# Kernel optimization log

Measured on AMD Instinct MI355X. Metric: run time of the kernel, lower is better.

## Reference

```python
import jax, jax.numpy as jnp
import numpy as np

HIDDEN = 1024
JOINTS = 21
IN_DIM = JOINTS * 3  # 63
BATCH = 64
SEQ = 512


def setup_inputs() -> dict:
    key = jax.random.key(0)
    ks = jax.random.split(key, 11)
    s = 0.02
    f32 = jnp.float32
    return {
        "real_seq": jax.random.normal(ks[0], (BATCH, SEQ, IN_DIM), f32),
        # PyTorch nn.GRU params (gates ordered r, z, n)
        "W_ih": jax.random.normal(ks[1], (3 * HIDDEN, IN_DIM), f32) * s,
        "W_hh": jax.random.normal(ks[2], (3 * HIDDEN, HIDDEN), f32) * s,
        "b_ih": jax.random.normal(ks[3], (3 * HIDDEN,), f32) * s,
        "b_hh": jax.random.normal(ks[4], (3 * HIDDEN,), f32) * s,
        # projector MLP (no nonlinearities in the original)
        "W1": jax.random.normal(ks[5], (HIDDEN, HIDDEN), f32) * s,
        "b1": jax.random.normal(ks[6], (HIDDEN,), f32) * s,
        "W2": jax.random.normal(ks[7], (HIDDEN, HIDDEN), f32) * s,
        "b2": jax.random.normal(ks[8], (HIDDEN,), f32) * s,
        "W3": jax.random.normal(ks[9], (IN_DIM, HIDDEN), f32) * s,
        "b3": jax.random.normal(ks[10], (IN_DIM,), f32) * s,
        "condition_length": 5,
        "ground_truth_length": 5,
    }


def _condition_list(seq_len, condition_length, ground_truth_length):
    gt = np.ones((100, ground_truth_length))
    co = np.zeros((100, condition_length))
    return np.concatenate((gt, co), 1).reshape(-1)[:seq_len]


def reference(real_seq, W_ih, W_hh, b_ih, b_hh, W1, b1, W2, b2, W3, b3,
              condition_length, ground_truth_length):
    B, T, D = real_seq.shape
    H = W_hh.shape[1]
    cond = jnp.asarray(_condition_list(T, condition_length, ground_truth_length),
                       dtype=real_seq.dtype)  # [T], static 1/0 teacher-forcing pattern

    h0 = jnp.zeros((B, H), real_seq.dtype)
    o0 = jnp.zeros((B, D), real_seq.dtype)
    xs = (jnp.transpose(real_seq, (1, 0, 2)), cond)  # time-major

    def step(carry, x):
        h, out = carry
        xt, c = x
        inp = jnp.where(c > 0.5, xt, out)  # teacher-forcing switch
        gi = inp @ W_ih.T + b_ih           # [B, 3H]
        gh = h @ W_hh.T + b_hh             # [B, 3H]
        i_r, i_z, i_n = jnp.split(gi, 3, axis=-1)
        h_r, h_z, h_n = jnp.split(gh, 3, axis=-1)
        r = jax.nn.sigmoid(i_r + h_r)
        z = jax.nn.sigmoid(i_z + h_z)
        n = jnp.tanh(i_n + r * h_n)
        h_new = (1.0 - z) * n + z * h
        lin = (h_new @ W1.T + b1) @ W2.T + b2
        out_new = inp + lin @ W3.T + b3    # residual velocities
        return (h_new, out_new), out_new

    _, outs = jax.lax.scan(step, (h0, o0), xs)  # outs: [T, B, D]
    return jnp.transpose(outs, (1, 0, 2)).reshape(B, T, D // 3, 3)
```

## Files before the change

### kernel.cpp

```cpp
#include <hip/hip_runtime.h>
#include <hip/hip_bf16.h>


#define HIDDEN 1024
#define INDIM  63
#define TSEQ   512
#define MB     16
#define NGRP   4
#define HB_DW  (MB * 512)

typedef __attribute__((ext_vector_type(8))) short bfrag8;
typedef __attribute__((ext_vector_type(4))) float ffrag4;
typedef __attribute__((ext_vector_type(4))) unsigned u32x4;
typedef unsigned long long ull;

#define MFMA_B16(a, b, c) __builtin_amdgcn_mfma_f32_16x16x32_bf16((a), (b), (c), 0, 0, 0)

#define GLOAD4(dst, ptr) \
  asm volatile("global_load_dwordx4 %0, %1, off sc0 sc1" \
               : "=v"(dst) : "v"(ptr) : "memory")

__device__ __forceinline__ short f2bf(float x) {
  __hip_bfloat16 b = __float2bfloat16(x);
  return __builtin_bit_cast(short, b);
}
__device__ __forceinline__ float bf2f(short s) {
  unsigned u = ((unsigned)(unsigned short)s) << 16;
  return __builtin_bit_cast(float, u);
}


__global__ void k_t1(const float* __restrict__ W2, const float* __restrict__ b1,
                     const float* __restrict__ b2, float* __restrict__ t1) {
  const int w = threadIdx.x >> 6, lane = threadIdx.x & 63;
  const int o = blockIdx.x * 4 + w;
  if (o >= HIDDEN) return;
  const float* row = W2 + (size_t)o * HIDDEN;
  float s = 0.f;
  for (int k = lane; k < HIDDEN; k += 64) s += row[k] * b1[k];
  for (int off = 32; off; off >>= 1) s += __shfl_down(s, off, 64);
  if (lane == 0) t1[o] = s + b2[o];
}

__global__ void k_bp(const float* __restrict__ W3, const float* __restrict__ t1,
                     const float* __restrict__ b3, float* __restrict__ bp) {
  const int w = threadIdx.x >> 6, lane = threadIdx.x & 63;
  for (int d = w; d < INDIM; d += 4) {
    const float* row = W3 + (size_t)d * HIDDEN;
    float s = 0.f;
    for (int k = lane; k < HIDDEN; k += 64) s += row[k] * t1[k];
    for (int off = 32; off; off >>= 1) s += __shfl_down(s, off, 64);
    if (lane == 0) bp[d] = s + b3[d];
  }
}

__global__ void k_gemm(const float* __restrict__ A, const float* __restrict__ B,
                       float* __restrict__ C, int M, int N, int K) {
  __shared__ float As[16][17], Bs[16][17];
  const int tx = threadIdx.x, ty = threadIdx.y;
  const int row = blockIdx.y * 16 + ty;
  const int col = blockIdx.x * 16 + tx;
  float acc = 0.f;
  for (int k0 = 0; k0 < K; k0 += 16) {
    As[ty][tx] = (row < M) ? A[(size_t)row * K + k0 + tx] : 0.f;
    Bs[ty][tx] = B[(size_t)(k0 + ty) * N + col];
    __syncthreads();
#pragma unroll
    for (int kk = 0; kk < 16; ++kk) acc += As[ty][kk] * Bs[kk][tx];
    __syncthreads();
  }
  if (row < M && col < N) C[(size_t)row * N + col] = acc;
}


__global__ __launch_bounds__(256, 1) void k_main(
    const float* __restrict__ X,
    const float* __restrict__ W_ih, const float* __restrict__ W_hh,
    const float* __restrict__ b_ih, const float* __restrict__ b_hh,
    const float* __restrict__ WpF, const float* __restrict__ bpF,
    const int* __restrict__ pCL, const int* __restrict__ pGT,
    unsigned* __restrict__ hb, unsigned* __restrict__ fl,
    float* __restrict__ OUT) {
  __shared__ short h_st[MB][HIDDEN + 8];
  __shared__ short inp_bf[MB][88];
  __shared__ float inp_f[MB][68];
  __shared__ float gt_z[MB][20], gt_hn[MB][20];
  __shared__ float gt_ir[MB][20], gt_iz[MB][20], gt_in[MB][20];
  __shared__ short htmp[MB][20];

  const int tid = threadIdx.x;
  const int w = tid >> 6;
  const int lane = tid & 63;
  const int c = lane & 15;
  const int quad = lane >> 4;
  const int g = blockIdx.x >> 6;
  const int j = blockIdx.x & 63;

  const int gtv = pGT[0];
  int period = pCL[0] + gtv;
  if (period < 1) period = 1;

  bfrag8 wB[32];
  bfrag8 wp[32];
  if (w < 3) {
    const float* wr = W_hh + ((size_t)w * HIDDEN + (size_t)j * 16 + c) * HIDDEN;
#pragma unroll
    for (int ks = 0; ks < 32; ++ks) {
      const float* p = wr + ks * 32 + quad * 8;
      bfrag8 f;
#pragma unroll
      for (int e = 0; e < 8; ++e) f[e] = f2bf(p[e]);
      wB[ks] = f;
    }
  } else {
#pragma unroll
    for (int gate = 0; gate < 3; ++gate) {
      const float* wr = W_ih + ((size_t)gate * HIDDEN + (size_t)j * 16 + c) * INDIM;
#pragma unroll
      for (int ks = 0; ks < 2; ++ks) {
        bfrag8 f;
#pragma unroll
        for (int e = 0; e < 8; ++e) {
          int k = ks * 32 + quad * 8 + e;
          f[e] = (k < INDIM) ? f2bf(wr[k]) : (short)0;
        }
        wB[gate * 2 + ks] = f;
      }
    }
  }
  const int dd = 16 * w + c;
  {
    const float* wr = WpF + (size_t)dd * HIDDEN;
#pragma unroll
    for (int ks = 0; ks < 32; ++ks) {
      bfrag8 f;
#pragma unroll
      for (int e = 0; e < 8; ++e)
        f[e] = (dd < INDIM) ? f2bf(wr[ks * 32 + quad * 8 + e]) : (short)0;
      wp[ks] = f;
    }
  }

  float bias_g;
  if (w == 0)      bias_g = b_ih[j * 16 + c] + b_hh[j * 16 + c];
  else if (w == 1) bias_g = b_ih[HIDDEN + j * 16 + c] + b_hh[HIDDEN + j * 16 + c];
  else if (w == 2) bias_g = b_hh[2 * HIDDEN + j * 16 + c];
  else             bias_g = b_ih[2 * HIDDEN + j * 16 + c];
  const float bp_l = (dd < INDIM) ? bpF[dd] : 0.f;

  for (int i = tid; i < MB * (HIDDEN + 8); i += 256) ((short*)h_st)[i] = 0;
  for (int i = tid; i < MB * 88; i += 256) ((short*)inp_bf)[i] = 0;
  for (int i = tid; i < MB * 68; i += 256) ((float*)inp_f)[i] = 0.f;

  unsigned* hb_g[2] = {hb + (size_t)g * HB_DW,
                       hb + (size_t)(NGRP + g) * HB_DW};
  unsigned* fg = fl + g * 64;
  const unsigned* fladdr = fg + (lane & 15) * 4;

  const int xrow = tid >> 4, xd0 = (tid & 15) * 4;
  float xp[4];
  if ((0 % period) < gtv) {
    const float* xr = X + ((size_t)(g * MB + xrow) * TSEQ + 0) * INDIM;
#pragma unroll
    for (int e = 0; e < 4; ++e) xp[e] = (xd0 + e < INDIM) ? xr[xd0 + e] : 0.f;
  }

  for (int t = 0; t < TSEQ; ++t) {
    const unsigned tg = (unsigned)(t + 1);
    const bool teach = ((t % period) < gtv);
    if (teach) {
#pragma unroll
      for (int e = 0; e < 4; ++e) {
        inp_f[xrow][xd0 + e] = xp[e];
        inp_bf[xrow][xd0 + e] = f2bf(xp[e]);
      }
    }
    __syncthreads();

    ffrag4 ghr;
    float hp[4];
    if (w < 3) {
      ffrag4 acc[4];
#pragma unroll
      for (int e = 0; e < 4; ++e) {
        acc[0][e] = bias_g; acc[1][e] = 0.f; acc[2][e] = 0.f; acc[3][e] = 0.f;
      }
#pragma unroll
      for (int ks = 0; ks < 32; ++ks) {
        const bfrag8 a = *(const bfrag8*)&h_st[c][ks * 32 + quad * 8];
        acc[ks & 3] = MFMA_B16(a, wB[ks], acc[ks & 3]);
      }
      ffrag4 gsum = acc[0] + acc[1] + acc[2] + acc[3];
      if (w == 1) {
#pragma unroll
        for (int i = 0; i < 4; ++i) gt_z[quad * 4 + i][c] = gsum[i];
      } else if (w == 2) {
#pragma unroll
        for (int i = 0; i < 4; ++i) gt_hn[quad * 4 + i][c] = gsum[i];
      } else {
        ghr = gsum;
#pragma unroll
        for (int i = 0; i < 4; ++i) hp[i] = bf2f(h_st[quad * 4 + i][j * 16 + c]);
      }
    } else {
      ffrag4 gir, giz, gin;
#pragma unroll
      for (int e = 0; e < 4; ++e) { gir[e] = 0.f; giz[e] = 0.f; gin[e] = bias_g; }
#pragma unroll
      for (int ks = 0; ks < 2; ++ks) {
        const bfrag8 a = *(const bfrag8*)&inp_bf[c][ks * 32 + quad * 8];
        gir = MFMA_B16(a, wB[0 + ks], gir);
        giz = MFMA_B16(a, wB[2 + ks], giz);
        gin = MFMA_B16(a, wB[4 + ks], gin);
      }
#pragma unroll
      for (int i = 0; i < 4; ++i) {
        gt_ir[quad * 4 + i][c] = gir[i];
        gt_iz[quad * 4 + i][c] = giz[i];
        gt_in[quad * 4 + i][c] = gin[i];
      }
    }
    __syncthreads();

    unsigned* hw = hb_g[t & 1];
    if (w == 0) {
#pragma unroll
      for (int i = 0; i < 4; ++i) {
        const int row = quad * 4 + i;
        float r = 1.f / (1.f + __expf(-(ghr[i] + gt_ir[row][c])));
        float z = 1.f / (1.f + __expf(-(gt_z[row][c] + gt_iz[row][c])));
        float n = tanhf(gt_in[row][c] + r * gt_hn[row][c]);
        htmp[row][c] = f2bf((1.f - z) * n + z * hp[i]);
      }
      asm volatile("" ::: "memory");
      const int r = lane >> 2, li = lane & 3, q4 = li * 4;
      ull pv = (ull)(unsigned short)htmp[r][q4 + 0] |
               ((ull)(unsigned short)htmp[r][q4 + 1] << 16) |
               ((ull)(unsigned short)htmp[r][q4 + 2] << 32) |
               ((ull)(unsigned short)htmp[r][q4 + 3] << 48);
      __hip_atomic_store((ull*)hw + (size_t)r * 256 + j * 4 + li, pv,
                         __ATOMIC_RELAXED, __HIP_MEMORY_SCOPE_SYSTEM);
      asm volatile("s_waitcnt vmcnt(0)" ::: "memory");
      if (lane == 0)
        __hip_atomic_store(&fg[j], tg, __ATOMIC_RELAXED,
                           __HIP_MEMORY_SCOPE_SYSTEM);
    }

    {
      const int tn = t + 1;
      if (tn < TSEQ && ((tn % period) < gtv)) {
        const float* xr = X + ((size_t)(g * MB + xrow) * TSEQ + tn) * INDIM;
#pragma unroll
        for (int e = 0; e < 4; ++e) xp[e] = (xd0 + e < INDIM) ? xr[xd0 + e] : 0.f;
      }
    }

    {
      for (;;) {
        u32x4 fv;
        GLOAD4(fv, fladdr);
        asm volatile("s_waitcnt vmcnt(0)" ::: "memory");
        __builtin_amdgcn_sched_barrier(0);
        const bool ok = fv[0] >= tg && fv[1] >= tg && fv[2] >= tg && fv[3] >= tg;
        if (__ballot(!ok) == 0ull) break;
        __builtin_amdgcn_s_sleep(1);
      }

      u32x4 v[8];
      const unsigned* gp = hw;
#pragma unroll
      for (int s = 0; s < 8; ++s) GLOAD4(v[s], gp + (size_t)(s * 256 + tid) * 4);
      asm volatile("s_waitcnt vmcnt(0)" ::: "memory");
      __builtin_amdgcn_sched_barrier(0);
#pragma unroll
      for (int s = 0; s < 8; ++s) {
        const int u = s * 256 + tid;
        const int row = u >> 7;
        const int col0 = (u & 127) * 8;
        *(u32x4*)&h_st[row][col0] = v[s];
      }
    }
    __syncthreads();

    const int wj = t & 63;
    const bool rep = (t + 1 < TSEQ) && !(((t + 1) % period) < gtv);
    if (rep || j == wj) {
      ffrag4 oa0, oa1;
#pragma unroll
      for (int e = 0; e < 4; ++e) { oa0[e] = bp_l; oa1[e] = 0.f; }
#pragma unroll
      for (int ks = 0; ks < 32; ++ks) {
        const bfrag8 a = *(const bfrag8*)&h_st[c][ks * 32 + quad * 8];
        if (ks & 1) oa1 = MFMA_B16(a, wp[ks], oa1);
        else        oa0 = MFMA_B16(a, wp[ks], oa0);
      }
      ffrag4 o = oa0 + oa1;
#pragma unroll
      for (int i = 0; i < 4; ++i) {
        const int row = quad * 4 + i;
        if (dd < INDIM) {
          float val = o[i] + inp_f[row][dd];
          if (j == wj) OUT[((size_t)(g * MB + row) * TSEQ + t) * INDIM + dd] = val;
          if (rep) { inp_f[row][dd] = val; inp_bf[row][dd] = f2bf(val); }
        } else if (rep) {
          inp_bf[row][dd] = 0;
        }
      }
    }
  }
}


extern "C" void kernel_launch(void* const* d_in, const int* in_sizes, int n_in,
                              void* d_out, int out_size, void* d_ws, size_t ws_size,
                              hipStream_t stream) {
  const float* X    = (const float*)d_in[0];
  const float* W_ih = (const float*)d_in[1];
  const float* W_hh = (const float*)d_in[2];
  const float* b_ih = (const float*)d_in[3];
  const float* b_hh = (const float*)d_in[4];
  const float* W1   = (const float*)d_in[5];
  const float* b1   = (const float*)d_in[6];
  const float* W2   = (const float*)d_in[7];
  const float* b2   = (const float*)d_in[8];
  const float* W3   = (const float*)d_in[9];
  const float* b3   = (const float*)d_in[10];
  const int* pCL    = (const int*)d_in[11];
  const int* pGT    = (const int*)d_in[12];
  float* OUT = (float*)d_out;

  char* ws = (char*)d_ws;
  float* bp = (float*)(ws + 1024);
  float* t1 = (float*)(ws + 2048);
  float* Wp = (float*)(ws + 8192);
  float* T2 = (float*)(ws + 270336);
  unsigned* hb = (unsigned*)(ws + 270336);
  unsigned* fl = (unsigned*)(ws + 270336 + 2 * NGRP * HB_DW * sizeof(unsigned));
  if (ws_size < 795 * 1024) return;

  k_t1<<<256, 256, 0, stream>>>(W2, b1, b2, t1);
  k_gemm<<<dim3(64, 4), dim3(16, 16), 0, stream>>>(W3, W2, T2, INDIM, HIDDEN, HIDDEN);
  k_gemm<<<dim3(64, 4), dim3(16, 16), 0, stream>>>(T2, W1, Wp, INDIM, HIDDEN, HIDDEN);
  k_bp<<<1, 256, 0, stream>>>(W3, t1, b3, bp);
  hipMemsetAsync(hb, 0,
                 (size_t)2 * NGRP * HB_DW * sizeof(unsigned) +
                     NGRP * 64 * sizeof(unsigned),
                 stream);
  k_main<<<256, 256, 0, stream>>>(X, W_ih, W_hh, b_ih, b_hh, Wp, bp, pCL, pGT,
                                  hb, fl, OUT);
}
```

Baseline: 3.483 ms.

## Split batch into eight groups and add XCD-local fast sync path with fallback

Result: slower. 12.75 ms (+266.0%).

```diff
diff --git a/kernel.cpp b/kernel.cpp
--- a/kernel.cpp
+++ b/kernel.cpp
@@ -5,20 +5,17 @@
 #define HIDDEN 1024
 #define INDIM  63
 #define TSEQ   512
-#define MB     16
-#define NGRP   4
-#define HB_DW  (MB * 512)
+#define MB     8
+#define GROUPS 8
+#define PAYDW  4096
 
 typedef __attribute__((ext_vector_type(8))) short bfrag8;
 typedef __attribute__((ext_vector_type(4))) float ffrag4;
 typedef __attribute__((ext_vector_type(4))) unsigned u32x4;
+typedef __attribute__((ext_vector_type(2))) unsigned u32x2;
 typedef unsigned long long ull;
 
 #define MFMA_B16(a, b, c) __builtin_amdgcn_mfma_f32_16x16x32_bf16((a), (b), (c), 0, 0, 0)
-
-#define GLOAD4(dst, ptr) \
-  asm volatile("global_load_dwordx4 %0, %1, off sc0 sc1" \
-               : "=v"(dst) : "v"(ptr) : "memory")
 
 __device__ __forceinline__ short f2bf(float x) {
   __hip_bfloat16 b = __float2bfloat16(x);
@@ -73,37 +70,68 @@
 }
 
 
-__global__ __launch_bounds__(256, 1) void k_main(
+__global__ __launch_bounds__(512, 2) void k_main(
     const float* __restrict__ X,
     const float* __restrict__ W_ih, const float* __restrict__ W_hh,
     const float* __restrict__ b_ih, const float* __restrict__ b_hh,
     const float* __restrict__ WpF, const float* __restrict__ bpF,
     const int* __restrict__ pCL, const int* __restrict__ pGT,
-    unsigned* __restrict__ hb, unsigned* __restrict__ fl,
-    float* __restrict__ OUT) {
-  __shared__ short h_st[MB][HIDDEN + 8];
-  __shared__ short inp_bf[MB][88];
-  __shared__ float inp_f[MB][68];
-  __shared__ float gt_z[MB][20], gt_hn[MB][20];
-  __shared__ float gt_ir[MB][20], gt_iz[MB][20], gt_in[MB][20];
-  __shared__ short htmp[MB][20];
+    unsigned* __restrict__ ctrl, unsigned* __restrict__ hbM,
+    unsigned* __restrict__ hbF, float* __restrict__ OUT) {
+  __shared__ short h_st[16][HIDDEN + 8];
+  __shared__ short inp_bf[16][88];
+  __shared__ float inp_f[16][68];
+  __shared__ float gt_z[2][16][20], gt_hn[2][16][20];
+  __shared__ float gt_ir[2][16][20], gt_iz[2][16][20], gt_in[2][16][20];
+  __shared__ short htmp[2][16][20];
 
   const int tid = threadIdx.x;
-  const int w = tid >> 6;
+  const int w8 = tid >> 6;
   const int lane = tid & 63;
+  const int sl = w8 >> 2;
+  const int ww = w8 & 3;
   const int c = lane & 15;
   const int quad = lane >> 4;
-  const int g = blockIdx.x >> 6;
-  const int j = blockIdx.x & 63;
+  const int bid = blockIdx.x;
+  const int g = bid & 7;
+  const int blockj = bid >> 3;
+  const int js = blockj * 2 + sl;
+
+  unsigned* flM = ctrl;
+  unsigned* xa  = ctrl + 512;
+  unsigned* vt  = ctrl + 768;
+  unsigned* dg  = ctrl + 1024;
+  unsigned* pw  = ctrl + 1056;
+  ull* ebc      = (ull*)(ctrl + 1344);
+  ull* flF      = (ull*)(ctrl + 1376);
+  ull* epoch    = (ull*)(ctrl + 2400);
+
+  unsigned* flMg = flM + g * 64;
+  ull*      flFg = flF + g * 64;
+  unsigned* dgg  = dg + g;
+
+  if (tid == 0) {
+    unsigned* pp = pw + g * 32 + blockj;
+    unsigned mk = 0xA5u;
+    asm volatile("global_store_dword %0, %1, off sc0" :: "v"(pp), "v"(mk) : "memory");
+    asm volatile("s_waitcnt vmcnt(0)" ::: "memory");
+    __hip_atomic_store(xa + g * 32 + blockj, 1u, __ATOMIC_RELAXED,
+                       __HIP_MEMORY_SCOPE_SYSTEM);
+    if (bid == 0) {
+      ull e = __hip_atomic_fetch_add(epoch, 1ull, __ATOMIC_RELAXED,
+                                     __HIP_MEMORY_SCOPE_SYSTEM);
+      __hip_atomic_store(ebc, (e << 1) | 1ull, __ATOMIC_RELAXED,
+                         __HIP_MEMORY_SCOPE_SYSTEM);
+    }
+  }
 
   const int gtv = pGT[0];
   int period = pCL[0] + gtv;
   if (period < 1) period = 1;
 
   bfrag8 wB[32];
-  bfrag8 wp[32];
-  if (w < 3) {
-    const float* wr = W_hh + ((size_t)w * HIDDEN + (size_t)j * 16 + c) * HIDDEN;
+  if (ww < 3) {
+    const float* wr = W_hh + ((size_t)ww * HIDDEN + (size_t)js * 16 + c) * HIDDEN;
 #pragma unroll
     for (int ks = 0; ks < 32; ++ks) {
       const float* p = wr + ks * 32 + quad * 8;
@@ -115,7 +143,7 @@
   } else {
 #pragma unroll
     for (int gate = 0; gate < 3; ++gate) {
-      const float* wr = W_ih + ((size_t)gate * HIDDEN + (size_t)j * 16 + c) * INDIM;
+      const float* wr = W_ih + ((size_t)gate * HIDDEN + (size_t)js * 16 + c) * INDIM;
 #pragma unroll
       for (int ks = 0; ks < 2; ++ks) {
         bfrag8 f;
@@ -128,8 +156,9 @@
       }
     }
   }
-  const int dd = 16 * w + c;
-  {
+  const int dd = 16 * w8 + c;
+  bfrag8 wp[32];
+  if (w8 < 4) {
     const float* wr = WpF + (size_t)dd * HIDDEN;
 #pragma unroll
     for (int ks = 0; ks < 32; ++ks) {
@@ -142,24 +171,60 @@
   }
 
   float bias_g;
-  if (w == 0)      bias_g = b_ih[j * 16 + c] + b_hh[j * 16 + c];
-  else if (w == 1) bias_g = b_ih[HIDDEN + j * 16 + c] + b_hh[HIDDEN + j * 16 + c];
-  else if (w == 2) bias_g = b_hh[2 * HIDDEN + j * 16 + c];
-  else             bias_g = b_ih[2 * HIDDEN + j * 16 + c];
-  const float bp_l = (dd < INDIM) ? bpF[dd] : 0.f;
-
-  for (int i = tid; i < MB * (HIDDEN + 8); i += 256) ((short*)h_st)[i] = 0;
-  for (int i = tid; i < MB * 88; i += 256) ((short*)inp_bf)[i] = 0;
-  for (int i = tid; i < MB * 68; i += 256) ((float*)inp_f)[i] = 0.f;
-
-  unsigned* hb_g[2] = {hb + (size_t)g * HB_DW,
-                       hb + (size_t)(NGRP + g) * HB_DW};
-  unsigned* fg = fl + g * 64;
-  const unsigned* fladdr = fg + (lane & 15) * 4;
+  if (ww == 0)      bias_g = b_ih[js * 16 + c] + b_hh[js * 16 + c];
+  else if (ww == 1) bias_g = b_ih[HIDDEN + js * 16 + c] + b_hh[HIDDEN + js * 16 + c];
+  else if (ww == 2) bias_g = b_hh[2 * HIDDEN + js * 16 + c];
+  else              bias_g = b_ih[2 * HIDDEN + js * 16 + c];
+  const float bp_l = (w8 < 4 && dd < INDIM) ? bpF[dd] : 0.f;
+
+  for (int i = tid; i < 16 * (HIDDEN + 8); i += 512) ((short*)h_st)[i] = 0;
+  for (int i = tid; i < 16 * 88; i += 512) ((short*)inp_bf)[i] = 0;
+  for (int i = tid; i < 16 * 68; i += 512) ((float*)inp_f)[i] = 0.f;
+
+  {
+    const unsigned* a = xa + g * 32 + (lane & 31);
+    while (__hip_atomic_load(a, __ATOMIC_RELAXED, __HIP_MEMORY_SCOPE_SYSTEM) == 0)
+      __builtin_amdgcn_s_sleep(2);
+  }
+  if (tid < 64) {
+    const unsigned* pp = pw + g * 32 + (lane & 31);
+    int okp = 0;
+    for (int it = 0; it < 64; ++it) {
+      unsigned v;
+      asm volatile("global_load_dword %0, %1, off sc0" : "=v"(v) : "v"(pp) : "memory");
+      asm volatile("s_waitcnt vmcnt(0)" ::: "memory");
+      __builtin_amdgcn_sched_barrier(0);
+      if (__ballot(v == 0) == 0ull) { okp = 1; break; }
+      __builtin_amdgcn_s_sleep(2);
+    }
+    if (lane == 0)
+      __hip_atomic_store(vt + g * 32 + blockj, okp ? 1u : 2u,
+                         __ATOMIC_RELAXED, __HIP_MEMORY_SCOPE_SYSTEM);
+  }
+  bool fast;
+  {
+    const unsigned* vv = vt + g * 32 + (lane & 31);
+    unsigned mv;
+    while ((mv = __hip_atomic_load(vv, __ATOMIC_RELAXED,
+                                   __HIP_MEMORY_SCOPE_SYSTEM)) == 0)
+      __builtin_amdgcn_s_sleep(2);
+    fast = (__ballot(mv != 1u) == 0ull);
+  }
+  ull ftg_base;
+  {
+    ull e;
+    while (((e = __hip_atomic_load(ebc, __ATOMIC_RELAXED,
+                                   __HIP_MEMORY_SCOPE_SYSTEM)) & 1ull) == 0)
+      __builtin_amdgcn_s_sleep(2);
+    ftg_base = (e >> 1) << 10;
+  }
+
+  unsigned* hbMg[2] = {hbM + g * PAYDW, hbM + (8 + g) * PAYDW};
+  unsigned* hbFg[2] = {hbF + g * PAYDW, hbF + (8 + g) * PAYDW};
 
   const int xrow = tid >> 4, xd0 = (tid & 15) * 4;
   float xp[4];
-  if ((0 % period) < gtv) {
+  if (tid < 128 && 0 < gtv) {
     const float* xr = X + ((size_t)(g * MB + xrow) * TSEQ + 0) * INDIM;
 #pragma unroll
     for (int e = 0; e < 4; ++e) xp[e] = (xd0 + e < INDIM) ? xr[xd0 + e] : 0.f;
@@ -167,8 +232,9 @@
 
   for (int t = 0; t < TSEQ; ++t) {
     const unsigned tg = (unsigned)(t + 1);
+    const ull ftg = ftg_base + (ull)tg;
     const bool teach = ((t % period) < gtv);
-    if (teach) {
+    if (teach && tid < 128) {
 #pragma unroll
       for (int e = 0; e < 4; ++e) {
         inp_f[xrow][xd0 + e] = xp[e];
@@ -179,7 +245,7 @@
 
     ffrag4 ghr;
     float hp[4];
-    if (w < 3) {
+    if (ww < 3) {
       ffrag4 acc[4];
 #pragma unroll
       for (int e = 0; e < 4; ++e) {
@@ -191,16 +257,16 @@
         acc[ks & 3] = MFMA_B16(a, wB[ks], acc[ks & 3]);
       }
       ffrag4 gsum = acc[0] + acc[1] + acc[2] + acc[3];
-      if (w == 1) {
-#pragma unroll
-        for (int i = 0; i < 4; ++i) gt_z[quad * 4 + i][c] = gsum[i];
-      } else if (w == 2) {
-#pragma unroll
-        for (int i = 0; i < 4; ++i) gt_hn[quad * 4 + i][c] = gsum[i];
+      if (ww == 1) {
+#pragma unroll
+        for (int i = 0; i < 4; ++i) gt_z[sl][quad * 4 + i][c] = gsum[i];
+      } else if (ww == 2) {
+#pragma unroll
+        for (int i = 0; i < 4; ++i) gt_hn[sl][quad * 4 + i][c] = gsum[i];
       } else {
         ghr = gsum;
 #pragma unroll
-        for (int i = 0; i < 4; ++i) hp[i] = bf2f(h_st[quad * 4 + i][j * 16 + c]);
+        for (int i = 0; i < 4; ++i) hp[i] = bf2f(h_st[quad * 4 + i][js * 16 + c]);
       }
     } else {
       ffrag4 gir, giz, gin;
@@ -215,38 +281,50 @@
       }
 #pragma unroll
       for (int i = 0; i < 4; ++i) {
-        gt_ir[quad * 4 + i][c] = gir[i];
-        gt_iz[quad * 4 + i][c] = giz[i];
-        gt_in[quad * 4 + i][c] = gin[i];
+        gt_ir[sl][quad * 4 + i][c] = gir[i];
+        gt_iz[sl][quad * 4 + i][c] = giz[i];
+        gt_in[sl][quad * 4 + i][c] = gin[i];
       }
     }
     __syncthreads();
 
-    unsigned* hw = hb_g[t & 1];
-    if (w == 0) {
+    unsigned* hwF = hbFg[t & 1];
+    unsigned* hwM = hbMg[t & 1];
+    unsigned pv = 0;
+    unsigned* pdM = hwM;
+    if (ww == 0) {
 #pragma unroll
       for (int i = 0; i < 4; ++i) {
         const int row = quad * 4 + i;
-        float r = 1.f / (1.f + __expf(-(ghr[i] + gt_ir[row][c])));
-        float z = 1.f / (1.f + __expf(-(gt_z[row][c] + gt_iz[row][c])));
-        float n = tanhf(gt_in[row][c] + r * gt_hn[row][c]);
-        htmp[row][c] = f2bf((1.f - z) * n + z * hp[i]);
+        float r = 1.f / (1.f + __expf(-(ghr[i] + gt_ir[sl][row][c])));
+        float z = 1.f / (1.f + __expf(-(gt_z[sl][row][c] + gt_iz[sl][row][c])));
+        float n = tanhf(gt_in[sl][row][c] + r * gt_hn[sl][row][c]);
+        htmp[sl][row][c] = f2bf((1.f - z) * n + z * hp[i]);
       }
       asm volatile("" ::: "memory");
-      const int r = lane >> 2, li = lane & 3, q4 = li * 4;
-      ull pv = (ull)(unsigned short)htmp[r][q4 + 0] |
-               ((ull)(unsigned short)htmp[r][q4 + 1] << 16) |
-               ((ull)(unsigned short)htmp[r][q4 + 2] << 32) |
-               ((ull)(unsigned short)htmp[r][q4 + 3] << 48);
-      __hip_atomic_store((ull*)hw + (size_t)r * 256 + j * 4 + li, pv,
-                         __ATOMIC_RELAXED, __HIP_MEMORY_SCOPE_SYSTEM);
-      asm volatile("s_waitcnt vmcnt(0)" ::: "memory");
-      if (lane == 0)
-        __hip_atomic_store(&fg[j], tg, __ATOMIC_RELAXED,
-                           __HIP_MEMORY_SCOPE_SYSTEM);
-    }
-
-    {
+      const int r = lane >> 3, cp = lane & 7;
+      pv = (unsigned)(unsigned short)htmp[sl][r][cp * 2] |
+           ((unsigned)(unsigned short)htmp[sl][r][cp * 2 + 1] << 16);
+      unsigned* pdF = hwF + r * 512 + js * 8 + cp;
+      pdM = hwM + r * 512 + js * 8 + cp;
+      if (fast) {
+        asm volatile("global_store_dword %0, %1, off sc0" :: "v"(pdF), "v"(pv) : "memory");
+        asm volatile("s_waitcnt vmcnt(0)" ::: "memory");
+        if (lane == 0) {
+          u32x2 fw; fw[0] = (unsigned)ftg; fw[1] = (unsigned)(ftg >> 32);
+          ull* fdst = flFg + js;
+          asm volatile("global_store_dwordx2 %0, %1, off sc0" :: "v"(fdst), "v"(fw) : "memory");
+        }
+      } else {
+        asm volatile("global_store_dword %0, %1, off sc0 sc1" :: "v"(pdM), "v"(pv) : "memory");
+        asm volatile("s_waitcnt vmcnt(0)" ::: "memory");
+        if (lane == 0)
+          __hip_atomic_store(&flMg[js], tg, __ATOMIC_RELAXED,
+                             __HIP_MEMORY_SCOPE_SYSTEM);
+      }
+    }
+
+    if (tid < 128) {
       const int tn = t + 1;
       if (tn < TSEQ && ((tn % period) < gtv)) {
         const float* xr = X + ((size_t)(g * MB + xrow) * TSEQ + tn) * INDIM;
@@ -255,36 +333,69 @@
       }
     }
 
-    {
+    if (fast) {
+      const ull* fa = flFg + lane;
+      int it = 0;
+      for (;;) {
+        u32x2 fw;
+        asm volatile("global_load_dwordx2 %0, %1, off sc0" : "=v"(fw) : "v"(fa) : "memory");
+        asm volatile("s_waitcnt vmcnt(0)" ::: "memory");
+        __builtin_amdgcn_sched_barrier(0);
+        ull fv = ((ull)fw[1] << 32) | (ull)fw[0];
+        if (__ballot(fv < ftg) == 0ull) break;
+        __builtin_amdgcn_s_sleep(1);
+        if (((++it) & 255) == 0) {
+          unsigned dv = __hip_atomic_load(dgg, __ATOMIC_RELAXED,
+                                          __HIP_MEMORY_SCOPE_SYSTEM);
+          if (dv || it > 16384) {
+            __hip_atomic_store(dgg, 1u, __ATOMIC_RELAXED, __HIP_MEMORY_SCOPE_SYSTEM);
+            fast = false;
+            if (ww == 0) {
+              asm volatile("global_store_dword %0, %1, off sc0 sc1" :: "v"(pdM), "v"(pv) : "memory");
+              asm volatile("s_waitcnt vmcnt(0)" ::: "memory");
+              if (lane == 0)
+                __hip_atomic_store(&flMg[js], tg, __ATOMIC_RELAXED,
+                                   __HIP_MEMORY_SCOPE_SYSTEM);
+            }
+            break;
+          }
+        }
+      }
+    }
+    if (!fast) {
+      const unsigned* fa = flMg + (lane & 15) * 4;
       for (;;) {
         u32x4 fv;
-        GLOAD4(fv, fladdr);
+        asm volatile("global_load_dwordx4 %0, %1, off sc0 sc1" : "=v"(fv) : "v"(fa) : "memory");
         asm volatile("s_waitcnt vmcnt(0)" ::: "memory");
         __builtin_amdgcn_sched_barrier(0);
-        const bool ok = fv[0] >= tg && fv[1] >= tg && fv[2] >= tg && fv[3] >= tg;
+        bool ok = fv[0] >= tg && fv[1] >= tg && fv[2] >= tg && fv[3] >= tg;
         if (__ballot(!ok) == 0ull) break;
         __builtin_amdgcn_s_sleep(1);
       }
-
-      u32x4 v[8];
-      const unsigned* gp = hw;
-#pragma unroll
-      for (int s = 0; s < 8; ++s) GLOAD4(v[s], gp + (size_t)(s * 256 + tid) * 4);
+    }
+
+    {
+      const unsigned* gp = (fast ? hwF : hwM) + (size_t)tid * 4;
+      u32x4 v0, v1;
+      if (fast) {
+        asm volatile("global_load_dwordx4 %0, %1, off sc0" : "=v"(v0) : "v"(gp) : "memory");
+        asm volatile("global_load_dwordx4 %0, %1, off sc0" : "=v"(v1) : "v"(gp + 2048) : "memory");
+      } else {
+        asm volatile("global_load_dwordx4 %0, %1, off sc0 sc1" : "=v"(v0) : "v"(gp) : "memory");
+        asm volatile("global_load_dwordx4 %0, %1, off sc0 sc1" : "=v"(v1) : "v"(gp + 2048) : "memory");
+      }
       asm volatile("s_waitcnt vmcnt(0)" ::: "memory");
       __builtin_amdgcn_sched_barrier(0);
-#pragma unroll
-      for (int s = 0; s < 8; ++s) {
-        const int u = s * 256 + tid;
-        const int row = u >> 7;
-        const int col0 = (u & 127) * 8;
-        *(u32x4*)&h_st[row][col0] = v[s];
-      }
+      *(u32x4*)&h_st[tid >> 7][(tid & 127) * 8] = v0;
+      const int u1 = tid + 512;
+      *(u32x4*)&h_st[u1 >> 7][(u1 & 127) * 8] = v1;
     }
     __syncthreads();
 
-    const int wj = t & 63;
+    const int wj = t & 31;
     const bool rep = (t + 1 < TSEQ) && !(((t + 1) % period) < gtv);
-    if (rep || j == wj) {
+    if (w8 < 4 && (rep || blockj == wj)) {
       ffrag4 oa0, oa1;
 #pragma unroll
       for (int e = 0; e < 4; ++e) { oa0[e] = bp_l; oa1[e] = 0.f; }
@@ -300,7 +411,8 @@
         const int row = quad * 4 + i;
         if (dd < INDIM) {
           float val = o[i] + inp_f[row][dd];
-          if (j == wj) OUT[((size_t)(g * MB + row) * TSEQ + t) * INDIM + dd] = val;
+          if (blockj == wj && row < MB)
+            OUT[((size_t)(g * MB + row) * TSEQ + t) * INDIM + dd] = val;
           if (rep) { inp_f[row][dd] = val; inp_bf[row][dd] = f2bf(val); }
         } else if (rep) {
           inp_bf[row][dd] = 0;
@@ -334,18 +446,16 @@
   float* t1 = (float*)(ws + 2048);
   float* Wp = (float*)(ws + 8192);
   float* T2 = (float*)(ws + 270336);
-  unsigned* hb = (unsigned*)(ws + 270336);
-  unsigned* fl = (unsigned*)(ws + 270336 + 2 * NGRP * HB_DW * sizeof(unsigned));
+  unsigned* hbM  = (unsigned*)(ws + 270336);
+  unsigned* ctrl = (unsigned*)(ws + 532480);
+  unsigned* hbF  = (unsigned*)(ws + 544768);
   if (ws_size < 795 * 1024) return;
 
   k_t1<<<256, 256, 0, stream>>>(W2, b1, b2, t1);
   k_gemm<<<dim3(64, 4), dim3(16, 16), 0, stream>>>(W3, W2, T2, INDIM, HIDDEN, HIDDEN);
   k_gemm<<<dim3(64, 4), dim3(16, 16), 0, stream>>>(T2, W1, Wp, INDIM, HIDDEN, HIDDEN);
   k_bp<<<1, 256, 0, stream>>>(W3, t1, b3, bp);
-  hipMemsetAsync(hb, 0,
-                 (size_t)2 * NGRP * HB_DW * sizeof(unsigned) +
-                     NGRP * 64 * sizeof(unsigned),
-                 stream);
-  k_main<<<256, 256, 0, stream>>>(X, W_ih, W_hh, b_ih, b_hh, Wp, bp, pCL, pGT,
-                                  hb, fl, OUT);
-}
+  hipMemsetAsync(ctrl, 0, 9600, stream);
+  k_main<<<256, 512, 0, stream>>>(X, W_ih, W_hh, b_ih, b_hh, Wp, bp, pCL, pGT,
+                                  ctrl, hbM, hbF, OUT);
+}
```
